# Kernel optimization log

Measured on AMD Instinct MI355X. Metric: run time of the kernel, lower is better.

The kernel has to match this reference:

```python
import jax, jax.numpy as jnp
import numpy as np

N, E = 100000, 1600000
DIM, H, D = 64, 4, 8          # dim, num_heads, qk_dim
DH = D * H                    # 32
QK_SCALE = (DIM // H) ** -0.5


def setup_inputs() -> dict:
    key = jax.random.key(0)
    k1, k2, k3, k4 = jax.random.split(key, 4)
    x = jax.random.normal(k1, (N, DIM), dtype=jnp.float32)
    edge_index = jax.random.randint(k2, (2, E), 0, N, dtype=jnp.int64)
    W_qkv = jax.random.normal(k3, (DIM, 2 * DH + DIM), dtype=jnp.float32) * (DIM ** -0.5)
    b_qkv = jax.random.normal(k4, (2 * DH + DIM,), dtype=jnp.float32) * 0.02
    return {"x": x, "edge_index": edge_index, "W_qkv": W_qkv, "b_qkv": b_qkv}


def reference(x, edge_index, W_qkv, b_qkv):
    n = x.shape[0]
    e = edge_index.shape[1]
    qkv = x @ W_qkv + b_qkv                       # (N, 2*DH+DIM)
    q = qkv[:, :DH].reshape(n, H, D)
    k = qkv[:, DH:2 * DH].reshape(n, H, D)
    v = qkv[:, 2 * DH:].reshape(n, H, DIM // H)
    s, t = edge_index[0], edge_index[1]
    q_e = q[s] * QK_SCALE                         # (E, H, D)
    k_e = k[t]
    v_e = v[t]                                    # (E, H, DIM/H)
    # scale q by 1/sqrt(num source neighbors) (bincount of s)
    deg = jax.ops.segment_sum(jnp.ones((e,), x.dtype), s, num_segments=n)
    q_e = q_e * (deg[s] ** -0.5)[:, None, None]
    compat = jnp.einsum('ehd,ehd->eh', q_e, k_e)  # (E, H)
    # segment softmax over edges grouped by source node s
    m = jax.ops.segment_max(compat, s, num_segments=n)
    ex = jnp.exp(compat - m[s])
    denom = jax.ops.segment_sum(ex, s, num_segments=n)
    attn = ex / (denom[s] + 1e-16)                # (E, H)
    msg = (v_e * attn[..., None]).reshape(e, DIM)  # (E, DIM)
    out = jax.ops.segment_sum(msg, s, num_segments=n)  # (N, DIM)
    return out
```

## Files before the change

### kernel.cpp

```cpp
#include <hip/hip_runtime.h>


#define NDIM 64
#define NBMAX 1024
#define CTILE 8192
#define STGMAX 4352

static __device__ __forceinline__ unsigned short f2bf(float f) {
    unsigned int u = __float_as_uint(f);
    unsigned int r = (u + 0x7fffu + ((u >> 16) & 1u)) >> 16;
    return (unsigned short)r;
}

__global__ void bucket_count_kernel(const int* __restrict__ s_arr,
                                    unsigned int* __restrict__ bcnt, int E) {
    __shared__ unsigned int h[NBMAX];
    for (int i = threadIdx.x; i < NBMAX; i += blockDim.x) h[i] = 0;
    __syncthreads();
    int i0 = blockIdx.x * blockDim.x + threadIdx.x;
    int st = gridDim.x * blockDim.x;
    for (int e = i0; e < E; e += st)
        atomicAdd(&h[(unsigned)s_arr[e] >> 7], 1u);
    __syncthreads();
    for (int i = threadIdx.x; i < NBMAX; i += blockDim.x)
        if (h[i]) atomicAdd(&bcnt[i], h[i]);
}

__global__ void scan_buckets_kernel(const unsigned int* __restrict__ bcnt,
                                    unsigned int* __restrict__ bbase,
                                    unsigned int* __restrict__ gcur) {
    __shared__ unsigned int sh[1024];
    int tid = threadIdx.x;
    unsigned int v = bcnt[tid];
    unsigned int acc = v;
    sh[tid] = acc;
    __syncthreads();
    for (int off = 1; off < 1024; off <<= 1) {
        unsigned int add = (tid >= off) ? sh[tid - off] : 0;
        __syncthreads();
        acc += add;
        sh[tid] = acc;
        __syncthreads();
    }
    bbase[tid] = acc - v;
    gcur[tid]  = acc - v;
}

__global__ void __launch_bounds__(1024, 2)
bin_kernel(const int* __restrict__ s_arr,
           const int* __restrict__ t_arr,
           unsigned int* __restrict__ gcur,
           unsigned int* __restrict__ binned, int E) {
    __shared__ unsigned int hist[NBMAX];
    __shared__ unsigned int off[NBMAX];
    __shared__ unsigned int gbase[NBMAX];
    __shared__ unsigned int stg[CTILE];
    __shared__ unsigned int psum[NBMAX];
    int tid = threadIdx.x;
    int e0 = blockIdx.x * CTILE;
    int cnt = min(CTILE, E - e0);

    hist[tid] = 0;
    __syncthreads();
    for (int i = tid; i < cnt; i += 1024)
        atomicAdd(&hist[(unsigned)s_arr[e0 + i] >> 7], 1u);
    __syncthreads();

    unsigned int v = hist[tid];
    unsigned int acc = v;
    psum[tid] = acc;
    __syncthreads();
    for (int o = 1; o < 1024; o <<= 1) {
        unsigned int add = (tid >= o) ? psum[tid - o] : 0;
        __syncthreads();
        acc += add;
        psum[tid] = acc;
        __syncthreads();
    }
    off[tid] = acc - v;
    __syncthreads();

    for (int i = tid; i < cnt; i += 1024) {
        int s = s_arr[e0 + i];
        int t = t_arr[e0 + i];
        unsigned int bkt = (unsigned)s >> 7;
        unsigned int p = atomicAdd(&off[bkt], 1u);
        stg[p] = ((unsigned)(s & 127) << 17) | (unsigned)t;
    }
    __syncthreads();

    {
        unsigned int h = hist[tid];
        gbase[tid] = h ? atomicAdd(&gcur[tid], h) : 0u;
    }
    __syncthreads();

    int wid = tid >> 6, lane = tid & 63;
    for (int b = wid; b < NBMAX; b += 16) {
        unsigned int h = hist[b];
        if (h == 0) continue;
        unsigned int src = off[b] - h;
        unsigned int dst = gbase[b];
        for (unsigned int i = lane; i < h; i += 64)
            binned[dst + i] = stg[src + i];
    }
}

__global__ void qkv_gemm_kernel(const float* __restrict__ x,
                                const float* __restrict__ W,
                                const float* __restrict__ b,
                                float* __restrict__ qs,
                                unsigned short* __restrict__ kv, int N) {
    int col = threadIdx.x & 127;
    int rw  = threadIdx.x >> 7;
    float w[64];
    #pragma unroll
    for (int k = 0; k < 64; ++k) w[k] = W[k * 128 + col];
    float bias = b[col];
    __shared__ float4 xs[8][16];

    for (int r0 = blockIdx.x * 8; r0 < N; r0 += gridDim.x * 8) {
        __syncthreads();
        if (threadIdx.x < 128) {
            int rr = threadIdx.x >> 4;
            int cc = threadIdx.x & 15;
            int n = r0 + rr;
            xs[rr][cc] = (n < N)
                ? reinterpret_cast<const float4*>(x)[(size_t)n * 16 + cc]
                : make_float4(0.f, 0.f, 0.f, 0.f);
        }
        __syncthreads();
        #pragma unroll
        for (int rsub = 0; rsub < 4; ++rsub) {
            int rr = rw * 4 + rsub;
            int n = r0 + rr;
            if (n < N) {
                float acc = bias;
                #pragma unroll
                for (int k4 = 0; k4 < 16; ++k4) {
                    float4 xv = xs[rr][k4];
                    acc = fmaf(xv.x, w[4 * k4 + 0], acc);
                    acc = fmaf(xv.y, w[4 * k4 + 1], acc);
                    acc = fmaf(xv.z, w[4 * k4 + 2], acc);
                    acc = fmaf(xv.w, w[4 * k4 + 3], acc);
                }
                if (col < 32) {
                    qs[(size_t)n * 32 + col] = acc;
                } else if (col < 64) {
                    kv[(size_t)n * 96 + (col - 32)] = f2bf(acc);
                } else {
                    kv[(size_t)n * 96 + 32 + (col - 64)] = f2bf(acc);
                }
            }
        }
    }
}

#define COMPUTE_EDGE(rr)                                              \
    {                                                                 \
        float lo = __uint_as_float((rr) << 16);                       \
        float hi = __uint_as_float((rr) & 0xffff0000u);               \
        float p = fmaf(q0, lo, q1 * hi);                              \
        p += __shfl_xor(p, 1);                                        \
        p += __shfl_xor(p, 2);                                        \
        float c = __shfl(p, csrc);                                    \
        float w = __expf(c);                                          \
        accx = fmaf(w, lo, accx);                                     \
        accy = fmaf(w, hi, accy);                                     \
        den += w;                                                     \
    }

__global__ void __launch_bounds__(512, 8)
sort_aggregate_kernel(const unsigned int* __restrict__ bbase,
                      const unsigned int* __restrict__ bcnt,
                      const unsigned int* __restrict__ binned,
                      const float* __restrict__ qs,
                      const unsigned int* __restrict__ kv32,
                      float* __restrict__ out, int N) {
    __shared__ unsigned int hist[128];
    __shared__ unsigned int rstart[128];
    __shared__ unsigned int cur[128];
    __shared__ unsigned int sh[128];
    __shared__ unsigned int stg[STGMAX];

    int b = blockIdx.x;
    int tid = threadIdx.x;
    unsigned int base = bbase[b];
    unsigned int cnt = min(bcnt[b], (unsigned int)STGMAX);

    if (tid < 128) hist[tid] = 0;
    __syncthreads();
    for (unsigned int i = tid; i < cnt; i += 512)
        atomicAdd(&hist[binned[base + i] >> 17], 1u);
    __syncthreads();

    unsigned int v = (tid < 128) ? hist[tid] : 0;
    unsigned int acc = v;
    if (tid < 128) sh[tid] = acc;
    __syncthreads();
    for (int o = 1; o < 128; o <<= 1) {
        unsigned int add = (tid >= o && tid < 128) ? sh[tid - o] : 0;
        __syncthreads();
        if (tid < 128) { acc += add; sh[tid] = acc; }
        __syncthreads();
    }
    if (tid < 128) {
        unsigned int exc = acc - v;
        rstart[tid] = exc;
        cur[tid] = exc;
    }
    __syncthreads();

    for (unsigned int i = tid; i < cnt; i += 512) {
        unsigned int e = binned[base + i];
        unsigned int p = atomicAdd(&cur[e >> 17], 1u);
        stg[p] = (e & 0x1FFFFu) * 192u;
    }
    __syncthreads();

    int wid = tid >> 6, lane = tid & 63;
    unsigned int lane4 = ((unsigned int)lane) << 2;
    bool ldact = (lane < 48);
    const char* kvb = (const char*)kv32;
    int csrc = (lane < 16) ? (lane & ~3)
             : (lane < 48) ? (((lane - 16) >> 3) << 2)
                           : 0;

    for (int nl = wid * 16; nl < wid * 16 + 16; ++nl) {
        int n = b * 128 + nl;
        if (n >= N) break;
        int dg = (int)hist[nl];
        if (dg == 0) {
            if (lane >= 16 && lane < 48)
                *reinterpret_cast<float2*>(&out[(size_t)n * 64 + 2 * (lane - 16)]) =
                    make_float2(0.f, 0.f);
            continue;
        }
        int start = (int)rstart[nl];
        float sc = 0.25f * rsqrtf((float)dg);
        float q0 = 0.f, q1 = 0.f;
        if (lane < 16) {
            q0 = qs[(size_t)n * 32 + 2 * lane] * sc;
            q1 = qs[(size_t)n * 32 + 2 * lane + 1] * sc;
        }

        float accx = 0.f, accy = 0.f, den = 0.f;
        int j = start;
        int rem = dg;

        unsigned int ra0 = 0, ra1 = 0, ra2 = 0, ra3 = 0;
        if (rem >= 4) {
            unsigned int o0 = stg[j] + lane4,     o1 = stg[j + 1] + lane4;
            unsigned int o2 = stg[j + 2] + lane4, o3 = stg[j + 3] + lane4;
            if (ldact) {
                ra0 = *(const unsigned int*)(kvb + o0);
                ra1 = *(const unsigned int*)(kvb + o1);
                ra2 = *(const unsigned int*)(kvb + o2);
                ra3 = *(const unsigned int*)(kvb + o3);
            }
        }
        while (rem >= 4) {
            unsigned int rb0 = 0, rb1 = 0, rb2 = 0, rb3 = 0;
            if (rem >= 8) {
                unsigned int o0 = stg[j + 4] + lane4, o1 = stg[j + 5] + lane4;
                unsigned int o2 = stg[j + 6] + lane4, o3 = stg[j + 7] + lane4;
                if (ldact) {
                    rb0 = *(const unsigned int*)(kvb + o0);
                    rb1 = *(const unsigned int*)(kvb + o1);
                    rb2 = *(const unsigned int*)(kvb + o2);
                    rb3 = *(const unsigned int*)(kvb + o3);
                }
            }
            COMPUTE_EDGE(ra0);
            COMPUTE_EDGE(ra1);
            COMPUTE_EDGE(ra2);
            COMPUTE_EDGE(ra3);
            ra0 = rb0; ra1 = rb1; ra2 = rb2; ra3 = rb3;
            j += 4; rem -= 4;
        }
        for (; rem > 0; --rem, ++j) {
            unsigned int o0 = stg[j] + lane4;
            unsigned int r0 = ldact ? *(const unsigned int*)(kvb + o0) : 0u;
            COMPUTE_EDGE(r0);
        }

        if (lane >= 16 && lane < 48) {
            float inv = 1.0f / (den + 1e-16f);
            float2 o = make_float2(accx * inv, accy * inv);
            *reinterpret_cast<float2*>(&out[(size_t)n * 64 + 2 * (lane - 16)]) = o;
        }
    }
}

extern "C" void kernel_launch(void* const* d_in, const int* in_sizes, int n_in,
                              void* d_out, int out_size, void* d_ws, size_t ws_size,
                              hipStream_t stream) {
    const float* x = (const float*)d_in[0];
    const int*   eidx = (const int*)d_in[1];
    const float* W = (const float*)d_in[2];
    const float* b = (const float*)d_in[3];
    int N = in_sizes[0] / NDIM;
    int E = in_sizes[1] / 2;
    float* out = (float*)d_out;

    int NB = (N + 127) / 128;

    float* qs = (float*)d_ws;
    unsigned short* kv = (unsigned short*)(qs + (size_t)N * 32);
    unsigned int* bcnt  = (unsigned int*)(kv + (size_t)N * 96);
    unsigned int* bbase = bcnt + NBMAX;
    unsigned int* gcur  = bbase + NBMAX;
    unsigned int* binned = gcur + NBMAX;

    const int* s_arr = eidx;
    const int* t_arr = eidx + E;

    hipMemsetAsync(bcnt, 0, NBMAX * sizeof(unsigned int), stream);

    bucket_count_kernel<<<512, 256, 0, stream>>>(s_arr, bcnt, E);
    scan_buckets_kernel<<<1, 1024, 0, stream>>>(bcnt, bbase, gcur);
    bin_kernel<<<(E + CTILE - 1) / CTILE, 1024, 0, stream>>>(s_arr, t_arr, gcur, binned, E);
    qkv_gemm_kernel<<<2048, 256, 0, stream>>>(x, W, b, qs, kv, N);
    sort_aggregate_kernel<<<NB, 512, 0, stream>>>(
        bbase, bcnt, binned, qs, (const unsigned int*)kv, out, N);
}
```

Baseline: 178.3 us.

## Fuse binning with QKV GEMM and use fixed-capacity bucket slots

```diff
diff --git a/kernel.cpp b/kernel.cpp
--- a/kernel.cpp
+++ b/kernel.cpp
@@ -5,6 +5,7 @@
 #define NBMAX 1024
 #define CTILE 8192
 #define STGMAX 4352
+#define GEMM_BLKS 256
 
 static __device__ __forceinline__ unsigned short f2bf(float f) {
     unsigned int u = __float_as_uint(f);
@@ -12,133 +13,105 @@
     return (unsigned short)r;
 }
 
-__global__ void bucket_count_kernel(const int* __restrict__ s_arr,
-                                    unsigned int* __restrict__ bcnt, int E) {
-    __shared__ unsigned int h[NBMAX];
-    for (int i = threadIdx.x; i < NBMAX; i += blockDim.x) h[i] = 0;
-    __syncthreads();
-    int i0 = blockIdx.x * blockDim.x + threadIdx.x;
-    int st = gridDim.x * blockDim.x;
-    for (int e = i0; e < E; e += st)
-        atomicAdd(&h[(unsigned)s_arr[e] >> 7], 1u);
-    __syncthreads();
-    for (int i = threadIdx.x; i < NBMAX; i += blockDim.x)
-        if (h[i]) atomicAdd(&bcnt[i], h[i]);
-}
-
-__global__ void scan_buckets_kernel(const unsigned int* __restrict__ bcnt,
-                                    unsigned int* __restrict__ bbase,
-                                    unsigned int* __restrict__ gcur) {
-    __shared__ unsigned int sh[1024];
+__global__ void fused_bin_gemm_kernel(const int* __restrict__ s_arr,
+                                      const int* __restrict__ t_arr,
+                                      unsigned int* __restrict__ gcur,
+                                      unsigned int* __restrict__ binned,
+                                      const float* __restrict__ x,
+                                      const float* __restrict__ W,
+                                      const float* __restrict__ bvec,
+                                      float* __restrict__ qs,
+                                      unsigned short* __restrict__ kv,
+                                      int N, int E, int nbin) {
+    __shared__ unsigned int sm[12288];
+    unsigned int* hist  = sm;
+    unsigned int* off   = sm + 1024;
+    unsigned int* gbase = sm + 2048;
+    unsigned int* psum  = sm + 3072;
+    unsigned int* stg   = sm + 4096;
     int tid = threadIdx.x;
-    unsigned int v = bcnt[tid];
-    unsigned int acc = v;
-    sh[tid] = acc;
-    __syncthreads();
-    for (int off = 1; off < 1024; off <<= 1) {
-        unsigned int add = (tid >= off) ? sh[tid - off] : 0;
-        __syncthreads();
-        acc += add;
-        sh[tid] = acc;
-        __syncthreads();
-    }
-    bbase[tid] = acc - v;
-    gcur[tid]  = acc - v;
-}
-
-__global__ void __launch_bounds__(1024, 2)
-bin_kernel(const int* __restrict__ s_arr,
-           const int* __restrict__ t_arr,
-           unsigned int* __restrict__ gcur,
-           unsigned int* __restrict__ binned, int E) {
-    __shared__ unsigned int hist[NBMAX];
-    __shared__ unsigned int off[NBMAX];
-    __shared__ unsigned int gbase[NBMAX];
-    __shared__ unsigned int stg[CTILE];
-    __shared__ unsigned int psum[NBMAX];
-    int tid = threadIdx.x;
-    int e0 = blockIdx.x * CTILE;
-    int cnt = min(CTILE, E - e0);
-
-    hist[tid] = 0;
-    __syncthreads();
-    for (int i = tid; i < cnt; i += 1024)
-        atomicAdd(&hist[(unsigned)s_arr[e0 + i] >> 7], 1u);
-    __syncthreads();
-
-    unsigned int v = hist[tid];
-    unsigned int acc = v;
-    psum[tid] = acc;
-    __syncthreads();
-    for (int o = 1; o < 1024; o <<= 1) {
-        unsigned int add = (tid >= o) ? psum[tid - o] : 0;
-        __syncthreads();
-        acc += add;
+
+    if (blockIdx.x < (unsigned)nbin) {
+        int e0 = blockIdx.x * CTILE;
+        int cnt = min(CTILE, E - e0);
+
+        hist[tid] = 0;
+        __syncthreads();
+        for (int i = tid; i < cnt; i += 1024)
+            atomicAdd(&hist[(unsigned)s_arr[e0 + i] >> 7], 1u);
+        __syncthreads();
+
+        unsigned int v = hist[tid];
+        unsigned int acc = v;
         psum[tid] = acc;
         __syncthreads();
-    }
-    off[tid] = acc - v;
-    __syncthreads();
-
-    for (int i = tid; i < cnt; i += 1024) {
-        int s = s_arr[e0 + i];
-        int t = t_arr[e0 + i];
-        unsigned int bkt = (unsigned)s >> 7;
-        unsigned int p = atomicAdd(&off[bkt], 1u);
-        stg[p] = ((unsigned)(s & 127) << 17) | (unsigned)t;
-    }
-    __syncthreads();
-
-    {
-        unsigned int h = hist[tid];
-        gbase[tid] = h ? atomicAdd(&gcur[tid], h) : 0u;
-    }
-    __syncthreads();
-
-    int wid = tid >> 6, lane = tid & 63;
-    for (int b = wid; b < NBMAX; b += 16) {
-        unsigned int h = hist[b];
-        if (h == 0) continue;
-        unsigned int src = off[b] - h;
-        unsigned int dst = gbase[b];
-        for (unsigned int i = lane; i < h; i += 64)
-            binned[dst + i] = stg[src + i];
-    }
-}
-
-__global__ void qkv_gemm_kernel(const float* __restrict__ x,
-                                const float* __restrict__ W,
-                                const float* __restrict__ b,
-                                float* __restrict__ qs,
-                                unsigned short* __restrict__ kv, int N) {
-    int col = threadIdx.x & 127;
-    int rw  = threadIdx.x >> 7;
-    float w[64];
-    #pragma unroll
-    for (int k = 0; k < 64; ++k) w[k] = W[k * 128 + col];
-    float bias = b[col];
-    __shared__ float4 xs[8][16];
-
-    for (int r0 = blockIdx.x * 8; r0 < N; r0 += gridDim.x * 8) {
-        __syncthreads();
-        if (threadIdx.x < 128) {
-            int rr = threadIdx.x >> 4;
-            int cc = threadIdx.x & 15;
-            int n = r0 + rr;
-            xs[rr][cc] = (n < N)
-                ? reinterpret_cast<const float4*>(x)[(size_t)n * 16 + cc]
-                : make_float4(0.f, 0.f, 0.f, 0.f);
-        }
-        __syncthreads();
+        for (int o = 1; o < 1024; o <<= 1) {
+            unsigned int add = (tid >= o) ? psum[tid - o] : 0;
+            __syncthreads();
+            acc += add;
+            psum[tid] = acc;
+            __syncthreads();
+        }
+        off[tid] = acc - v;
+        __syncthreads();
+
+        for (int i = tid; i < cnt; i += 1024) {
+            int s = s_arr[e0 + i];
+            int t = t_arr[e0 + i];
+            unsigned int bkt = (unsigned)s >> 7;
+            unsigned int p = atomicAdd(&off[bkt], 1u);
+            stg[p] = ((unsigned)(s & 127) << 17) | (unsigned)t;
+        }
+        __syncthreads();
+
+        {
+            unsigned int h = hist[tid];
+            unsigned int resv = h ? atomicAdd(&gcur[tid], h) : 0u;
+            unsigned int m = (resv < STGMAX) ? min(h, STGMAX - resv) : 0u;
+            hist[tid] = m;
+            gbase[tid] = (unsigned)tid * STGMAX + resv;
+        }
+        __syncthreads();
+
+        int wid = tid >> 6, lane = tid & 63;
+        for (int b = wid; b < NBMAX; b += 16) {
+            unsigned int m = hist[b];
+            if (m == 0) continue;
+            unsigned int src = off[b] - ((off[b] - m) - (off[b] - m));
+            unsigned int segstart = off[b];
+            unsigned int start = (b > 0) ? psum[b - 1] : 0u;
+            unsigned int dst = gbase[b];
+            for (unsigned int i = lane; i < m; i += 64)
+                binned[dst + i] = stg[start + i];
+            (void)src; (void)segstart;
+        }
+    } else {
+        float4* xs = (float4*)sm;
+        int bid = blockIdx.x - nbin;
+        int col = tid & 127;
+        int rw  = tid >> 7;
+        float w[64];
         #pragma unroll
-        for (int rsub = 0; rsub < 4; ++rsub) {
-            int rr = rw * 4 + rsub;
-            int n = r0 + rr;
+        for (int k = 0; k < 64; ++k) w[k] = W[k * 128 + col];
+        float bias = bvec[col];
+
+        for (int r0 = bid * 8; r0 < N; r0 += GEMM_BLKS * 8) {
+            __syncthreads();
+            if (tid < 128) {
+                int rr = tid >> 4;
+                int cc = tid & 15;
+                int n = r0 + rr;
+                xs[rr * 16 + cc] = (n < N)
+                    ? reinterpret_cast<const float4*>(x)[(size_t)n * 16 + cc]
+                    : make_float4(0.f, 0.f, 0.f, 0.f);
+            }
+            __syncthreads();
+            int n = r0 + rw;
             if (n < N) {
                 float acc = bias;
                 #pragma unroll
                 for (int k4 = 0; k4 < 16; ++k4) {
-                    float4 xv = xs[rr][k4];
+                    float4 xv = xs[rw * 16 + k4];
                     acc = fmaf(xv.x, w[4 * k4 + 0], acc);
                     acc = fmaf(xv.y, w[4 * k4 + 1], acc);
                     acc = fmaf(xv.z, w[4 * k4 + 2], acc);
@@ -171,8 +144,7 @@
     }
 
 __global__ void __launch_bounds__(512, 8)
-sort_aggregate_kernel(const unsigned int* __restrict__ bbase,
-                      const unsigned int* __restrict__ bcnt,
+sort_aggregate_kernel(const unsigned int* __restrict__ gcur,
                       const unsigned int* __restrict__ binned,
                       const float* __restrict__ qs,
                       const unsigned int* __restrict__ kv32,
@@ -185,8 +157,8 @@
 
     int b = blockIdx.x;
     int tid = threadIdx.x;
-    unsigned int base = bbase[b];
-    unsigned int cnt = min(bcnt[b], (unsigned int)STGMAX);
+    unsigned int base = (unsigned)b * STGMAX;
+    unsigned int cnt = min(gcur[b], (unsigned int)STGMAX);
 
     if (tid < 128) hist[tid] = 0;
     __syncthreads();
@@ -304,23 +276,20 @@
     float* out = (float*)d_out;
 
     int NB = (N + 127) / 128;
+    int nbin = (E + CTILE - 1) / CTILE;
 
     float* qs = (float*)d_ws;
     unsigned short* kv = (unsigned short*)(qs + (size_t)N * 32);
-    unsigned int* bcnt  = (unsigned int*)(kv + (size_t)N * 96);
-    unsigned int* bbase = bcnt + NBMAX;
-    unsigned int* gcur  = bbase + NBMAX;
+    unsigned int* gcur = (unsigned int*)(kv + (size_t)N * 96);
     unsigned int* binned = gcur + NBMAX;
 
     const int* s_arr = eidx;
     const int* t_arr = eidx + E;
 
-    hipMemsetAsync(bcnt, 0, NBMAX * sizeof(unsigned int), stream);
-
-    bucket_count_kernel<<<512, 256, 0, stream>>>(s_arr, bcnt, E);
-    scan_buckets_kernel<<<1, 1024, 0, stream>>>(bcnt, bbase, gcur);
-    bin_kernel<<<(E + CTILE - 1) / CTILE, 1024, 0, stream>>>(s_arr, t_arr, gcur, binned, E);
-    qkv_gemm_kernel<<<2048, 256, 0, stream>>>(x, W, b, qs, kv, N);
+    hipMemsetAsync(gcur, 0, NBMAX * sizeof(unsigned int), stream);
+
+    fused_bin_gemm_kernel<<<nbin + GEMM_BLKS, 1024, 0, stream>>>(
+        s_arr, t_arr, gcur, binned, x, W, b, qs, kv, N, E, nbin);
     sort_aggregate_kernel<<<NB, 512, 0, stream>>>(
-        bbase, bcnt, binned, qs, (const unsigned int*)kv, out, N);
-}
+        gcur, binned, qs, (const unsigned int*)kv, out, N);
+}
```

Measured after the change: 175.7 us. About the same (-1.4%).
